# Kernel optimization log

Hardware: AMD Instinct MI355X
Metric: run time of the kernel (lower is better)

Reference implementation:

```python
import jax, jax.numpy as jnp
import numpy as np

B, H = 128, 128          # batch_size must equal hidden_dim (see torch cat semantics)
IMG_DIM, TXT_DIM = 1024, 1024
N_EDGES = 32768


def setup_inputs() -> dict:
    key = jax.random.key(0)
    k_img, k_txt, k_e, k_w1, k_w2 = jax.random.split(key, 5)
    img_features = jax.random.normal(k_img, (B, IMG_DIM), dtype=jnp.float32)
    text_features = jax.random.normal(k_txt, (B, TXT_DIM), dtype=jnp.float32)
    # unique (source, target) edges so scatter-set is deterministic
    lin = jax.random.choice(k_e, IMG_DIM * TXT_DIM, shape=(N_EDGES,), replace=False)
    src = (lin // TXT_DIM).astype(jnp.int32)
    tgt = (lin % TXT_DIM).astype(jnp.int32)
    # causal_attention_net params: Linear(2H, H) -> ReLU -> Linear(H, 1) -> Sigmoid
    W1 = jax.random.normal(k_w1, (H, 2 * H), dtype=jnp.float32) / np.sqrt(2 * H)
    b1 = jnp.zeros((H,), dtype=jnp.float32)
    w2 = jax.random.normal(k_w2, (H,), dtype=jnp.float32) / np.sqrt(H)
    b2 = jnp.zeros((), dtype=jnp.float32)
    return {"img_features": img_features, "text_features": text_features,
            "src": src, "tgt": tgt, "W1": W1, "b1": b1, "w2": w2, "b2": b2}


def reference(img_features, text_features, src, tgt, W1, b1, w2, b2):
    batch_size, img_dim = img_features.shape
    _, text_dim = text_features.shape
    # per-edge gather of feature COLUMNS: [E, B] each -> concat [E, 2B] (B == H)
    pairs = jnp.concatenate([img_features[:, src].T, text_features[:, tgt].T], axis=1)
    h = jax.nn.relu(pairs @ W1.T + b1)           # [E, H]
    a = jax.nn.sigmoid(h @ w2 + b2)              # [E] scalar attention per edge
    # scatter into dense sparse-pattern attention matrix, broadcast over batch
    A = jnp.zeros((batch_size, img_dim, text_dim), dtype=img_features.dtype)
    A = A.at[:, src, tgt].set(a)                 # [B, I, T]
    attended_img = jnp.einsum('bit,bt->bi', A, text_features)   # [B, I]
    attended_text = jnp.einsum('bit,bi->bt', A, img_features)   # [B, T]
    return (attended_img, attended_text)
```

## Files before the change

### kernel.cpp

```cpp
#include <hip/hip_runtime.h>
#include <math.h>

#define BD   128
#define NCOL 1024
#define NE   32768
#define CAP  128
#define CNT_STRIDE 16

__global__ __launch_bounds__(256) void prep_kernel(
    const float* __restrict__ img, const float* __restrict__ text,
    const int* __restrict__ src, const int* __restrict__ tgt,
    const float* __restrict__ W1, const float* __restrict__ b1,
    float* __restrict__ HimgT, float* __restrict__ HtxtT,
    float* __restrict__ imgT, float* __restrict__ textT,
    int* __restrict__ cnt,
    int* __restrict__ list_src, int* __restrict__ list_tgt)
{
    __shared__ __align__(16) float Wl[64 * 129];
    __shared__ __align__(16) float Sl[128 * 8];
    const int blk = blockIdx.x, tid = threadIdx.x;

    if (blk < 256) {
        const int side = blk >> 7;
        const int i0 = (blk & 127) * 8;
        const float* S = side ? text : img;
        float* Dst = side ? HtxtT : HimgT;
        const int soff = side * 128;

        {
            int b = tid >> 1, q = tid & 1;
            ((float4*)Sl)[tid] = *(const float4*)(S + b * 1024 + i0 + q * 4);
        }
        const int h = tid & 127, iq = tid >> 7;
        float acc[4] = {0.f, 0.f, 0.f, 0.f};
        #pragma unroll
        for (int half = 0; half < 2; half++) {
            __syncthreads();
            for (int idx = tid; idx < 8192; idx += 256) {
                int hh = idx >> 6, bb = idx & 63;
                Wl[bb * 129 + hh] = W1[hh * 256 + soff + half * 64 + bb];
            }
            __syncthreads();
            #pragma unroll 8
            for (int bb = 0; bb < 64; bb++) {
                int b = half * 64 + bb;
                float w = Wl[bb * 129 + h];
                float4 s4 = *(const float4*)(Sl + b * 8 + iq * 4);
                acc[0] += s4.x * w; acc[1] += s4.y * w;
                acc[2] += s4.z * w; acc[3] += s4.w * w;
            }
        }
        float bias = side ? 0.f : b1[h];
        #pragma unroll
        for (int r = 0; r < 4; r++)
            Dst[(i0 + iq * 4 + r) * 128 + h] = acc[r] + bias;
    } else if (blk < 512) {
        float (*lds)[33] = (float(*)[33])Wl;
        const int t = blk - 256;
        const float* S = (t < 128) ? img : text;
        float* D = (t < 128) ? imgT : textT;
        const int tile = t & 127;
        const int rt = tile >> 5, ct = tile & 31;
        const int x = tid & 31, y = tid >> 5;
        #pragma unroll
        for (int k = 0; k < 4; k++) {
            int r = y + k * 8;
            lds[r][x] = S[(rt * 32 + r) * 1024 + ct * 32 + x];
        }
        __syncthreads();
        #pragma unroll
        for (int k = 0; k < 4; k++) {
            int r = y + k * 8;
            D[(ct * 32 + r) * 128 + rt * 32 + x] = lds[x][r];
        }
    } else {
        const int e = (blk - 512) * 256 + tid;
        const int s0 = src[e], t0 = tgt[e];
        int p = atomicAdd(&cnt[s0 * CNT_STRIDE], 1);
        if (p < CAP) list_src[s0 * CAP + p] = e;
        int q = atomicAdd(&cnt[(1024 + t0) * CNT_STRIDE], 1);
        if (q < CAP) list_tgt[t0 * CAP + q] = e;
    }
}

__global__ __launch_bounds__(256) void edge_kernel(
    const int* __restrict__ src, const int* __restrict__ tgt,
    const float* __restrict__ HimgT, const float* __restrict__ HtxtT,
    const float* __restrict__ w2, const float* __restrict__ b2,
    float* __restrict__ a_e)
{
    const int lane = threadIdx.x & 63;
    const int u = lane & 15, sub = lane >> 4;
    const int wid = blockIdx.x * 4 + (threadIdx.x >> 6);
    const float4 wa = *(const float4*)(w2 + u * 8);
    const float4 wb = *(const float4*)(w2 + u * 8 + 4);
    const float b2v = b2[0];

    #pragma unroll
    for (int j = 0; j < 2; j++) {
        const int e = wid * 8 + j * 4 + sub;
        const int s0 = src[e], t0 = tgt[e];
        const float4* Hi = (const float4*)(HimgT + s0 * 128) + u * 2;
        const float4* Ht = (const float4*)(HtxtT + t0 * 128) + u * 2;
        float4 h0 = Hi[0], h1 = Hi[1];
        float4 g0 = Ht[0], g1 = Ht[1];
        float x;
        x  = fmaxf(h0.x + g0.x, 0.f) * wa.x;
        x += fmaxf(h0.y + g0.y, 0.f) * wa.y;
        x += fmaxf(h0.z + g0.z, 0.f) * wa.z;
        x += fmaxf(h0.w + g0.w, 0.f) * wa.w;
        x += fmaxf(h1.x + g1.x, 0.f) * wb.x;
        x += fmaxf(h1.y + g1.y, 0.f) * wb.y;
        x += fmaxf(h1.z + g1.z, 0.f) * wb.z;
        x += fmaxf(h1.w + g1.w, 0.f) * wb.w;
        #pragma unroll
        for (int off = 1; off < 16; off <<= 1)
            x += __shfl_xor(x, off, 64);
        if (u == 0)
            a_e[e] = 1.f / (1.f + expf(-(x + b2v)));
    }
}

__global__ __launch_bounds__(128) void gather_kernel(
    const int* __restrict__ src, const int* __restrict__ tgt,
    const float* __restrict__ a_e,
    const int* __restrict__ cnt,
    const int* __restrict__ list_src, const int* __restrict__ list_tgt,
    const float* __restrict__ imgT, const float* __restrict__ textT,
    float* __restrict__ out)
{
    __shared__ float avl[CAP];
    __shared__ int   ol[CAP];
    const int blk = blockIdx.x, b = threadIdx.x;
    const int side = blk >> 10, c = blk & 1023;
    int n = cnt[(side * 1024 + c) * CNT_STRIDE];
    n = min(n, CAP);
    const int* lst = (side ? list_tgt : list_src) + c * CAP;
    const int* oth = side ? src : tgt;
    const float* T = side ? imgT : textT;

    if (b < n) {
        int e = lst[b];
        ol[b]  = oth[e];
        avl[b] = a_e[e];
    }
    __syncthreads();

    float acc0 = 0.f, acc1 = 0.f;
    int p = 0;
    for (; p + 1 < n; p += 2) {
        acc0 += avl[p]     * T[ol[p]     * 128 + b];
        acc1 += avl[p + 1] * T[ol[p + 1] * 128 + b];
    }
    if (p < n) acc0 += avl[p] * T[ol[p] * 128 + b];

    out[side * (BD * NCOL) + b * 1024 + c] = acc0 + acc1;
}

extern "C" void kernel_launch(void* const* d_in, const int* in_sizes, int n_in,
                              void* d_out, int out_size, void* d_ws, size_t ws_size,
                              hipStream_t stream)
{
    const float* img  = (const float*)d_in[0];
    const float* text = (const float*)d_in[1];
    const int*   src  = (const int*)  d_in[2];
    const int*   tgt  = (const int*)  d_in[3];
    const float* W1   = (const float*)d_in[4];
    const float* b1   = (const float*)d_in[5];
    const float* w2   = (const float*)d_in[6];
    const float* b2   = (const float*)d_in[7];
    float* out = (float*)d_out;

    float* HimgT  = (float*)d_ws;
    float* HtxtT  = HimgT + 131072;
    float* imgT   = HtxtT + 131072;
    float* textT  = imgT  + 131072;
    float* a_e    = textT + 131072;
    int* cnt      = (int*)(a_e + 32768);
    int* list_src = cnt + 2048 * CNT_STRIDE;
    int* list_tgt = list_src + 1024 * CAP;

    hipMemsetAsync(cnt, 0, 2048 * CNT_STRIDE * sizeof(int), stream);
    prep_kernel<<<640, 256, 0, stream>>>(img, text, src, tgt, W1, b1,
                                         HimgT, HtxtT, imgT, textT,
                                         cnt, list_src, list_tgt);
    edge_kernel<<<1024, 256, 0, stream>>>(src, tgt, HimgT, HtxtT, w2, b2, a_e);
    gather_kernel<<<2048, 128, 0, stream>>>(src, tgt, a_e, cnt,
                                            list_src, list_tgt,
                                            imgT, textT, out);
}
```

Baseline: 94.43 us.

## Fuse edge attention into gather kernel and bucket edges via LDS atomics

```diff
diff --git a/kernel.cpp b/kernel.cpp
--- a/kernel.cpp
+++ b/kernel.cpp
@@ -5,7 +5,6 @@
 #define NCOL 1024
 #define NE   32768
 #define CAP  128
-#define CNT_STRIDE 16
 
 __global__ __launch_bounds__(256) void prep_kernel(
     const float* __restrict__ img, const float* __restrict__ text,
@@ -74,58 +73,45 @@
             D[(ct * 32 + r) * 128 + rt * 32 + x] = lds[x][r];
         }
     } else {
-        const int e = (blk - 512) * 256 + tid;
-        const int s0 = src[e], t0 = tgt[e];
-        int p = atomicAdd(&cnt[s0 * CNT_STRIDE], 1);
-        if (p < CAP) list_src[s0 * CAP + p] = e;
-        int q = atomicAdd(&cnt[(1024 + t0) * CNT_STRIDE], 1);
-        if (q < CAP) list_tgt[t0 * CAP + q] = e;
+        int* lc = (int*)Sl;
+        const int fb = blk - 512;
+        const int side = fb >> 5;
+        const int base = (fb & 31) * 32;
+        const int* E = side ? tgt : src;
+        int* list = side ? list_tgt : list_src;
+
+        if (tid < 32) lc[tid] = 0;
+        __syncthreads();
+
+        #pragma unroll 4
+        for (int it = 0; it < 32; it++) {
+            const int e0 = it * 1024 + tid * 4;
+            int4 v = *(const int4*)(E + e0);
+            int c;
+            c = v.x - base;
+            if ((unsigned)c < 32u) { int s = atomicAdd(&lc[c], 1);
+                if (s < CAP) list[(base + c) * CAP + s] = e0; }
+            c = v.y - base;
+            if ((unsigned)c < 32u) { int s = atomicAdd(&lc[c], 1);
+                if (s < CAP) list[(base + c) * CAP + s] = e0 + 1; }
+            c = v.z - base;
+            if ((unsigned)c < 32u) { int s = atomicAdd(&lc[c], 1);
+                if (s < CAP) list[(base + c) * CAP + s] = e0 + 2; }
+            c = v.w - base;
+            if ((unsigned)c < 32u) { int s = atomicAdd(&lc[c], 1);
+                if (s < CAP) list[(base + c) * CAP + s] = e0 + 3; }
+        }
+        __syncthreads();
+        if (tid < 32) cnt[side * 1024 + base + tid] = min(lc[tid], CAP);
     }
 }
 
-__global__ __launch_bounds__(256) void edge_kernel(
+__global__ __launch_bounds__(128) void gather_kernel(
     const int* __restrict__ src, const int* __restrict__ tgt,
+    const int* __restrict__ cnt,
+    const int* __restrict__ list_src, const int* __restrict__ list_tgt,
     const float* __restrict__ HimgT, const float* __restrict__ HtxtT,
     const float* __restrict__ w2, const float* __restrict__ b2,
-    float* __restrict__ a_e)
-{
-    const int lane = threadIdx.x & 63;
-    const int u = lane & 15, sub = lane >> 4;
-    const int wid = blockIdx.x * 4 + (threadIdx.x >> 6);
-    const float4 wa = *(const float4*)(w2 + u * 8);
-    const float4 wb = *(const float4*)(w2 + u * 8 + 4);
-    const float b2v = b2[0];
-
-    #pragma unroll
-    for (int j = 0; j < 2; j++) {
-        const int e = wid * 8 + j * 4 + sub;
-        const int s0 = src[e], t0 = tgt[e];
-        const float4* Hi = (const float4*)(HimgT + s0 * 128) + u * 2;
-        const float4* Ht = (const float4*)(HtxtT + t0 * 128) + u * 2;
-        float4 h0 = Hi[0], h1 = Hi[1];
-        float4 g0 = Ht[0], g1 = Ht[1];
-        float x;
-        x  = fmaxf(h0.x + g0.x, 0.f) * wa.x;
-        x += fmaxf(h0.y + g0.y, 0.f) * wa.y;
-        x += fmaxf(h0.z + g0.z, 0.f) * wa.z;
-        x += fmaxf(h0.w + g0.w, 0.f) * wa.w;
-        x += fmaxf(h1.x + g1.x, 0.f) * wb.x;
-        x += fmaxf(h1.y + g1.y, 0.f) * wb.y;
-        x += fmaxf(h1.z + g1.z, 0.f) * wb.z;
-        x += fmaxf(h1.w + g1.w, 0.f) * wb.w;
-        #pragma unroll
-        for (int off = 1; off < 16; off <<= 1)
-            x += __shfl_xor(x, off, 64);
-        if (u == 0)
-            a_e[e] = 1.f / (1.f + expf(-(x + b2v)));
-    }
-}
-
-__global__ __launch_bounds__(128) void gather_kernel(
-    const int* __restrict__ src, const int* __restrict__ tgt,
-    const float* __restrict__ a_e,
-    const int* __restrict__ cnt,
-    const int* __restrict__ list_src, const int* __restrict__ list_tgt,
     const float* __restrict__ imgT, const float* __restrict__ textT,
     float* __restrict__ out)
 {
@@ -133,16 +119,44 @@
     __shared__ int   ol[CAP];
     const int blk = blockIdx.x, b = threadIdx.x;
     const int side = blk >> 10, c = blk & 1023;
-    int n = cnt[(side * 1024 + c) * CNT_STRIDE];
-    n = min(n, CAP);
+    int n = cnt[side * 1024 + c];
     const int* lst = (side ? list_tgt : list_src) + c * CAP;
     const int* oth = side ? src : tgt;
-    const float* T = side ? imgT : textT;
-
-    if (b < n) {
-        int e = lst[b];
-        ol[b]  = oth[e];
-        avl[b] = a_e[e];
+    const float* Hown = (side ? HtxtT : HimgT) + c * 128;
+    const float* Hoth = side ? HimgT : HtxtT;
+    const float* T    = side ? imgT : textT;
+
+    if (b < n)
+        ol[b] = oth[lst[b]];
+    __syncthreads();
+
+    {
+        const int u = b & 15;
+        const int group = (b >> 6) * 4 + ((b & 63) >> 4);
+        const float4 wa = *(const float4*)(w2 + u * 8);
+        const float4 wb = *(const float4*)(w2 + u * 8 + 4);
+        const float4 o0 = *(const float4*)(Hown + u * 8);
+        const float4 o1 = *(const float4*)(Hown + u * 8 + 4);
+        const float b2v = b2[0];
+        for (int p = group; p < n; p += 8) {
+            const float* Hr = Hoth + ol[p] * 128 + u * 8;
+            float4 g0 = *(const float4*)(Hr);
+            float4 g1 = *(const float4*)(Hr + 4);
+            float x;
+            x  = fmaxf(o0.x + g0.x, 0.f) * wa.x;
+            x += fmaxf(o0.y + g0.y, 0.f) * wa.y;
+            x += fmaxf(o0.z + g0.z, 0.f) * wa.z;
+            x += fmaxf(o0.w + g0.w, 0.f) * wa.w;
+            x += fmaxf(o1.x + g1.x, 0.f) * wb.x;
+            x += fmaxf(o1.y + g1.y, 0.f) * wb.y;
+            x += fmaxf(o1.z + g1.z, 0.f) * wb.z;
+            x += fmaxf(o1.w + g1.w, 0.f) * wb.w;
+            #pragma unroll
+            for (int off = 1; off < 16; off <<= 1)
+                x += __shfl_xor(x, off, 64);
+            if (u == 0)
+                avl[p] = 1.f / (1.f + expf(-(x + b2v)));
+        }
     }
     __syncthreads();
 
@@ -175,17 +189,15 @@
     float* HtxtT  = HimgT + 131072;
     float* imgT   = HtxtT + 131072;
     float* textT  = imgT  + 131072;
-    float* a_e    = textT + 131072;
-    int* cnt      = (int*)(a_e + 32768);
-    int* list_src = cnt + 2048 * CNT_STRIDE;
+    int* cnt      = (int*)(textT + 131072);
+    int* list_src = cnt + 2048;
     int* list_tgt = list_src + 1024 * CAP;
 
-    hipMemsetAsync(cnt, 0, 2048 * CNT_STRIDE * sizeof(int), stream);
-    prep_kernel<<<640, 256, 0, stream>>>(img, text, src, tgt, W1, b1,
+    prep_kernel<<<576, 256, 0, stream>>>(img, text, src, tgt, W1, b1,
                                          HimgT, HtxtT, imgT, textT,
                                          cnt, list_src, list_tgt);
-    edge_kernel<<<1024, 256, 0, stream>>>(src, tgt, HimgT, HtxtT, w2, b2, a_e);
-    gather_kernel<<<2048, 128, 0, stream>>>(src, tgt, a_e, cnt,
+    gather_kernel<<<2048, 128, 0, stream>>>(src, tgt, cnt,
                                             list_src, list_tgt,
+                                            HimgT, HtxtT, w2, b2,
                                             imgT, textT, out);
 }
```

Measured after the change: 97.15 us. 1.03x slower.

## Build edge bucket lists with per-block LDS atomics and drop the memset

Applied to the files above, without the earlier changes.

```diff
diff --git a/kernel.cpp b/kernel.cpp
--- a/kernel.cpp
+++ b/kernel.cpp
@@ -5,7 +5,6 @@
 #define NCOL 1024
 #define NE   32768
 #define CAP  128
-#define CNT_STRIDE 16
 
 __global__ __launch_bounds__(256) void prep_kernel(
     const float* __restrict__ img, const float* __restrict__ text,
@@ -74,12 +73,36 @@
             D[(ct * 32 + r) * 128 + rt * 32 + x] = lds[x][r];
         }
     } else {
-        const int e = (blk - 512) * 256 + tid;
-        const int s0 = src[e], t0 = tgt[e];
-        int p = atomicAdd(&cnt[s0 * CNT_STRIDE], 1);
-        if (p < CAP) list_src[s0 * CAP + p] = e;
-        int q = atomicAdd(&cnt[(1024 + t0) * CNT_STRIDE], 1);
-        if (q < CAP) list_tgt[t0 * CAP + q] = e;
+        int* lc = (int*)Sl;
+        const int fb = blk - 512;
+        const int side = fb >> 5;
+        const int base = (fb & 31) * 32;
+        const int* E = side ? tgt : src;
+        int* list = side ? list_tgt : list_src;
+
+        if (tid < 32) lc[tid] = 0;
+        __syncthreads();
+
+        #pragma unroll 4
+        for (int it = 0; it < 32; it++) {
+            const int e0 = it * 1024 + tid * 4;
+            int4 v = *(const int4*)(E + e0);
+            int c;
+            c = v.x - base;
+            if ((unsigned)c < 32u) { int s = atomicAdd(&lc[c], 1);
+                if (s < CAP) list[(base + c) * CAP + s] = e0; }
+            c = v.y - base;
+            if ((unsigned)c < 32u) { int s = atomicAdd(&lc[c], 1);
+                if (s < CAP) list[(base + c) * CAP + s] = e0 + 1; }
+            c = v.z - base;
+            if ((unsigned)c < 32u) { int s = atomicAdd(&lc[c], 1);
+                if (s < CAP) list[(base + c) * CAP + s] = e0 + 2; }
+            c = v.w - base;
+            if ((unsigned)c < 32u) { int s = atomicAdd(&lc[c], 1);
+                if (s < CAP) list[(base + c) * CAP + s] = e0 + 3; }
+        }
+        __syncthreads();
+        if (tid < 32) cnt[side * 1024 + base + tid] = min(lc[tid], CAP);
     }
 }
 
@@ -92,33 +115,30 @@
     const int lane = threadIdx.x & 63;
     const int u = lane & 15, sub = lane >> 4;
     const int wid = blockIdx.x * 4 + (threadIdx.x >> 6);
+    const int e = wid * 4 + sub;
     const float4 wa = *(const float4*)(w2 + u * 8);
     const float4 wb = *(const float4*)(w2 + u * 8 + 4);
     const float b2v = b2[0];
 
+    const int s0 = src[e], t0 = tgt[e];
+    const float4* Hi = (const float4*)(HimgT + s0 * 128) + u * 2;
+    const float4* Ht = (const float4*)(HtxtT + t0 * 128) + u * 2;
+    float4 h0 = Hi[0], h1 = Hi[1];
+    float4 g0 = Ht[0], g1 = Ht[1];
+    float x;
+    x  = fmaxf(h0.x + g0.x, 0.f) * wa.x;
+    x += fmaxf(h0.y + g0.y, 0.f) * wa.y;
+    x += fmaxf(h0.z + g0.z, 0.f) * wa.z;
+    x += fmaxf(h0.w + g0.w, 0.f) * wa.w;
+    x += fmaxf(h1.x + g1.x, 0.f) * wb.x;
+    x += fmaxf(h1.y + g1.y, 0.f) * wb.y;
+    x += fmaxf(h1.z + g1.z, 0.f) * wb.z;
+    x += fmaxf(h1.w + g1.w, 0.f) * wb.w;
     #pragma unroll
-    for (int j = 0; j < 2; j++) {
-        const int e = wid * 8 + j * 4 + sub;
-        const int s0 = src[e], t0 = tgt[e];
-        const float4* Hi = (const float4*)(HimgT + s0 * 128) + u * 2;
-        const float4* Ht = (const float4*)(HtxtT + t0 * 128) + u * 2;
-        float4 h0 = Hi[0], h1 = Hi[1];
-        float4 g0 = Ht[0], g1 = Ht[1];
-        float x;
-        x  = fmaxf(h0.x + g0.x, 0.f) * wa.x;
-        x += fmaxf(h0.y + g0.y, 0.f) * wa.y;
-        x += fmaxf(h0.z + g0.z, 0.f) * wa.z;
-        x += fmaxf(h0.w + g0.w, 0.f) * wa.w;
-        x += fmaxf(h1.x + g1.x, 0.f) * wb.x;
-        x += fmaxf(h1.y + g1.y, 0.f) * wb.y;
-        x += fmaxf(h1.z + g1.z, 0.f) * wb.z;
-        x += fmaxf(h1.w + g1.w, 0.f) * wb.w;
-        #pragma unroll
-        for (int off = 1; off < 16; off <<= 1)
-            x += __shfl_xor(x, off, 64);
-        if (u == 0)
-            a_e[e] = 1.f / (1.f + expf(-(x + b2v)));
-    }
+    for (int off = 1; off < 16; off <<= 1)
+        x += __shfl_xor(x, off, 64);
+    if (u == 0)
+        a_e[e] = 1.f / (1.f + expf(-(x + b2v)));
 }
 
 __global__ __launch_bounds__(128) void gather_kernel(
@@ -133,8 +153,7 @@
     __shared__ int   ol[CAP];
     const int blk = blockIdx.x, b = threadIdx.x;
     const int side = blk >> 10, c = blk & 1023;
-    int n = cnt[(side * 1024 + c) * CNT_STRIDE];
-    n = min(n, CAP);
+    int n = cnt[side * 1024 + c];
     const int* lst = (side ? list_tgt : list_src) + c * CAP;
     const int* oth = side ? src : tgt;
     const float* T = side ? imgT : textT;
@@ -177,14 +196,13 @@
     float* textT  = imgT  + 131072;
     float* a_e    = textT + 131072;
     int* cnt      = (int*)(a_e + 32768);
-    int* list_src = cnt + 2048 * CNT_STRIDE;
+    int* list_src = cnt + 2048;
     int* list_tgt = list_src + 1024 * CAP;
 
-    hipMemsetAsync(cnt, 0, 2048 * CNT_STRIDE * sizeof(int), stream);
-    prep_kernel<<<640, 256, 0, stream>>>(img, text, src, tgt, W1, b1,
+    prep_kernel<<<576, 256, 0, stream>>>(img, text, src, tgt, W1, b1,
                                          HimgT, HtxtT, imgT, textT,
                                          cnt, list_src, list_tgt);
-    edge_kernel<<<1024, 256, 0, stream>>>(src, tgt, HimgT, HtxtT, w2, b2, a_e);
+    edge_kernel<<<2048, 256, 0, stream>>>(src, tgt, HimgT, HtxtT, w2, b2, a_e);
     gather_kernel<<<2048, 128, 0, stream>>>(src, tgt, a_e, cnt,
                                             list_src, list_tgt,
                                             imgT, textT, out);
```

Measured after the change: 98.59 us. 4.4% more time.
